# Kernel tuning notes

Measured on AMD Instinct MI355X. Metric: run time of the kernel, lower is better.

## Reference

```python
import jax, jax.numpy as jnp
import numpy as np

IN_F = 1024
OUT_F = 1024

def setup_inputs() -> dict:
    key = jax.random.key(0)
    ks = jax.random.split(key, 7)
    s = 1.0 / np.sqrt(IN_F)
    x = jax.random.normal(ks[0], (4, 2048, IN_F), dtype=jnp.float32)
    Wq = jax.random.uniform(ks[1], (OUT_F, IN_F), jnp.float32, -s, s)
    bq = jax.random.uniform(ks[2], (OUT_F,), jnp.float32, -s, s)
    Wk = jax.random.uniform(ks[3], (OUT_F, IN_F), jnp.float32, -s, s)
    bk = jax.random.uniform(ks[4], (OUT_F,), jnp.float32, -s, s)
    Wv = jax.random.uniform(ks[5], (OUT_F, IN_F), jnp.float32, -s, s)
    bv = jax.random.uniform(ks[6], (OUT_F,), jnp.float32, -s, s)
    return {"x": x, "Wq": Wq, "bq": bq, "Wk": Wk, "bk": bk, "Wv": Wv, "bv": bv}

def reference(x, Wq, bq, Wk, bk, Wv, bv):
    # Projector: ReLU(Linear(x))
    q = jax.nn.relu(jnp.einsum('bsd,od->bso', x, Wq) + bq)  # [B,S,O]
    k = jax.nn.relu(jnp.einsum('bsd,od->bso', x, Wk) + bk)
    v = jax.nn.relu(jnp.einsum('bsd,od->bso', x, Wv) + bv)
    logits = jnp.einsum('bio,bko->bik', q, k)  # unscaled QK^T, [B,S,S]
    scores = jax.nn.softmax(logits, axis=-1)
    out = jnp.einsum('bik,bko->bio', scores, v)
    return out
```

## Files before the change

### kernel.cpp

```cpp
#include <hip/hip_runtime.h>
#include <hip/hip_bf16.h>


#define SEQ 2048
#define DIM 1024
#define NB 4
#define MTOT (NB * SEQ)

typedef __attribute__((ext_vector_type(8))) short frag_ab;
typedef __attribute__((ext_vector_type(16))) float frag_c16;

__device__ __forceinline__ ushort f2bf(float f) {
    union { float f; unsigned u; } x; x.f = f;
    unsigned r = x.u + 0x7fffu + ((x.u >> 16) & 1u);
    return (ushort)(r >> 16);
}

typedef __attribute__((address_space(1))) const unsigned int guint;
typedef __attribute__((address_space(3))) unsigned int luint;

__device__ __forceinline__ void gld_lds16(const void* g, void* l) {
    __builtin_amdgcn_global_load_lds((guint*)g, (luint*)l, 16, 0, 0);
}

__device__ __forceinline__ void gemm_tiles(
    const ushort* __restrict__ A, size_t lda,
    const ushort* __restrict__ B, size_t ldb, int K,
    ushort* As, ushort* Bs, frag_c16 (&acc)[2][2])
{
    const int tid  = threadIdx.x;
    const int wave = tid >> 6;
    const int lane = tid & 63;
    const int l32  = lane & 31;
    const int half = lane >> 5;
    const int sr = wave * 16 + (lane >> 2);
    const int sc = lane & 3;
    const int wm = (wave & 1) * 64;
    const int wn = (wave >> 1) * 64;

    for (int k0 = 0; k0 < K; k0 += 32) {
        #pragma unroll
        for (int j = 0; j < 2; ++j) {
            int row = j * 64 + sr;
            int cg  = sc ^ ((row >> 1) & 3);
            ushort* la = As + (j * 64 + wave * 16) * 32;
            ushort* lb = Bs + (j * 64 + wave * 16) * 32;
            gld_lds16(A + (size_t)row * lda + k0 + cg * 8, la);
            gld_lds16(B + (size_t)row * ldb + k0 + cg * 8, lb);
        }
        __syncthreads();
        frag_ab af[2][2], bfr[2][2];
        #pragma unroll
        for (int mi = 0; mi < 2; ++mi) {
            int row = wm + mi * 32 + l32;
            int sw = (row >> 1) & 3;
            #pragma unroll
            for (int h = 0; h < 2; ++h) {
                int c = (h * 2 + half) ^ sw;
                af[mi][h] = *(const frag_ab*)&As[row * 32 + c * 8];
            }
        }
        #pragma unroll
        for (int ni = 0; ni < 2; ++ni) {
            int row = wn + ni * 32 + l32;
            int sw = (row >> 1) & 3;
            #pragma unroll
            for (int h = 0; h < 2; ++h) {
                int c = (h * 2 + half) ^ sw;
                bfr[ni][h] = *(const frag_ab*)&Bs[row * 32 + c * 8];
            }
        }
        #pragma unroll
        for (int h = 0; h < 2; ++h)
            #pragma unroll
            for (int mi = 0; mi < 2; ++mi)
                #pragma unroll
                for (int ni = 0; ni < 2; ++ni)
                    acc[mi][ni] = __builtin_amdgcn_mfma_f32_32x32x16_bf16(
                        af[mi][h], bfr[ni][h], acc[mi][ni], 0, 0, 0);
        __syncthreads();
    }
}


#define NX4 (MTOT * DIM / 4)
#define NW4 (DIM * DIM / 4)
__global__ __launch_bounds__(256) void cvt_kernel(
    const float* __restrict__ x,
    const float* __restrict__ Wq, const float* __restrict__ Wk,
    const float* __restrict__ Wv,
    ushort* __restrict__ xb, ushort* __restrict__ Wb)
{
    size_t i = (size_t)blockIdx.x * 256 + threadIdx.x;
    const float* src; ushort* dst; size_t idx;
    if (i < NX4) { src = x; dst = xb; idx = i; }
    else {
        size_t j = i - NX4;
        int w = (int)(j >> 18);
        idx = j & (NW4 - 1);
        src = w == 0 ? Wq : (w == 1 ? Wk : Wv);
        dst = Wb + (size_t)w * DIM * DIM;
    }
    float4 f = ((const float4*)src)[idx];
    ushort4 u; u.x = f2bf(f.x); u.y = f2bf(f.y); u.z = f2bf(f.z); u.w = f2bf(f.w);
    ((ushort4*)dst)[idx] = u;
}

__global__ __launch_bounds__(256) void qkv_kernel(
    const ushort* __restrict__ xb, const ushort* __restrict__ Wb,
    const float* __restrict__ bq, const float* __restrict__ bk,
    const float* __restrict__ bv,
    ushort* __restrict__ q, ushort* __restrict__ k, ushort* __restrict__ v)
{
    const float* bias; ushort* out;
    if (blockIdx.z == 0)      { bias = bq; out = q; }
    else if (blockIdx.z == 1) { bias = bk; out = k; }
    else                      { bias = bv; out = v; }
    const ushort* W = Wb + (size_t)blockIdx.z * DIM * DIM;

    __shared__ ushort As[128 * 32];
    __shared__ ushort Bs[128 * 32];

    const int tid  = threadIdx.x;
    const int wave = tid >> 6;
    const int lane = tid & 63;
    const int l32  = lane & 31;
    const int half = lane >> 5;
    const int m0 = blockIdx.x * 128;
    const int n0 = blockIdx.y * 128;
    const int wm = (wave & 1) * 64;
    const int wn = (wave >> 1) * 64;

    frag_c16 acc[2][2] = {};
    gemm_tiles(xb + (size_t)m0 * DIM, DIM, W + (size_t)n0 * DIM, DIM, DIM,
               As, Bs, acc);

    #pragma unroll
    for (int ni = 0; ni < 2; ++ni) {
        int col = n0 + wn + ni * 32 + l32;
        float bb = bias[col];
        #pragma unroll
        for (int mi = 0; mi < 2; ++mi)
            #pragma unroll
            for (int r = 0; r < 16; ++r) {
                int row = m0 + wm + mi * 32 + (r & 3) + 8 * (r >> 2) + 4 * half;
                float val = acc[mi][ni][r] + bb;
                val = val > 0.0f ? val : 0.0f;
                out[(size_t)row * DIM + col] = f2bf(val);
            }
    }
}

__global__ __launch_bounds__(256) void transpose_v(
    const ushort* __restrict__ v, ushort* __restrict__ vt)
{
    __shared__ ushort T[64][72];
    const int bz = blockIdx.z;
    const int s0 = blockIdx.x * 64;
    const int o0 = blockIdx.y * 64;
    const int t  = threadIdx.x;

    #pragma unroll
    for (int p = 0; p < 4; ++p) {
        int sl = p * 16 + (t >> 4);
        int o4 = (t & 15) * 4;
        ushort4 u = *(const ushort4*)&v[(size_t)(bz * SEQ + s0 + sl) * DIM + o0 + o4];
        *(ushort4*)&T[sl][o4] = u;
    }
    __syncthreads();
    #pragma unroll
    for (int p = 0; p < 4; ++p) {
        int ol = p * 16 + (t >> 4);
        int s4 = (t & 15) * 4;
        ushort4 u;
        u.x = T[s4 + 0][ol]; u.y = T[s4 + 1][ol];
        u.z = T[s4 + 2][ol]; u.w = T[s4 + 3][ol];
        *(ushort4*)&vt[(size_t)(bz * DIM + o0 + ol) * SEQ + s0 + s4] = u;
    }
}

__global__ __launch_bounds__(256) void qk_kernel(
    const ushort* __restrict__ q, const ushort* __restrict__ kk,
    float* __restrict__ logits)
{
    __shared__ ushort As[128 * 32];
    __shared__ ushort Bs[128 * 32];

    const int tid  = threadIdx.x;
    const int wave = tid >> 6;
    const int lane = tid & 63;
    const int l32  = lane & 31;
    const int half = lane >> 5;
    const int bz = blockIdx.z;
    const int m0 = blockIdx.x * 128;
    const int n0 = blockIdx.y * 128;
    const int wm = (wave & 1) * 64;
    const int wn = (wave >> 1) * 64;
    const size_t base = (size_t)bz * SEQ;

    frag_c16 acc[2][2] = {};
    gemm_tiles(q + (base + m0) * DIM, DIM, kk + (base + n0) * DIM, DIM, DIM,
               As, Bs, acc);

    #pragma unroll
    for (int mi = 0; mi < 2; ++mi)
        #pragma unroll
        for (int r = 0; r < 16; ++r) {
            int row = m0 + wm + mi * 32 + (r & 3) + 8 * (r >> 2) + 4 * half;
            #pragma unroll
            for (int ni = 0; ni < 2; ++ni) {
                int col = n0 + wn + ni * 32 + l32;
                logits[(base + row) * SEQ + col] = acc[mi][ni][r];
            }
        }
}

__global__ __launch_bounds__(256) void softmax_kernel(float* __restrict__ logits)
{
    float* p = logits + (size_t)blockIdx.x * SEQ;
    const int t = threadIdx.x;
    const int wave = t >> 6, lane = t & 63;

    float4 a = ((const float4*)p)[t];
    float4 b = ((const float4*)p)[t + 256];

    float m = fmaxf(fmaxf(fmaxf(a.x, a.y), fmaxf(a.z, a.w)),
                    fmaxf(fmaxf(b.x, b.y), fmaxf(b.z, b.w)));
    #pragma unroll
    for (int off = 32; off; off >>= 1) m = fmaxf(m, __shfl_down(m, off, 64));

    __shared__ float red[4];
    if (lane == 0) red[wave] = m;
    __syncthreads();
    m = fmaxf(fmaxf(red[0], red[1]), fmaxf(red[2], red[3]));

    a.x = __expf(a.x - m); a.y = __expf(a.y - m);
    a.z = __expf(a.z - m); a.w = __expf(a.w - m);
    b.x = __expf(b.x - m); b.y = __expf(b.y - m);
    b.z = __expf(b.z - m); b.w = __expf(b.w - m);

    float s = (a.x + a.y + a.z + a.w) + (b.x + b.y + b.z + b.w);
    #pragma unroll
    for (int off = 32; off; off >>= 1) s += __shfl_down(s, off, 64);
    __syncthreads();
    if (lane == 0) red[wave] = s;
    __syncthreads();
    s = red[0] + red[1] + red[2] + red[3];
    float inv = 1.0f / s;

    ushort* o = (ushort*)p;
    ushort4 u0, u1;
    u0.x = f2bf(a.x * inv); u0.y = f2bf(a.y * inv);
    u0.z = f2bf(a.z * inv); u0.w = f2bf(a.w * inv);
    u1.x = f2bf(b.x * inv); u1.y = f2bf(b.y * inv);
    u1.z = f2bf(b.z * inv); u1.w = f2bf(b.w * inv);
    ((ushort4*)o)[t]       = u0;
    ((ushort4*)o)[t + 256] = u1;
}

__global__ __launch_bounds__(256) void pv_kernel(
    const ushort* __restrict__ probs, const ushort* __restrict__ vt,
    float* __restrict__ out)
{
    __shared__ ushort As[128 * 32];
    __shared__ ushort Bs[128 * 32];

    const int tid  = threadIdx.x;
    const int wave = tid >> 6;
    const int lane = tid & 63;
    const int l32  = lane & 31;
    const int half = lane >> 5;
    const int bz = blockIdx.z;
    const int m0 = blockIdx.x * 128;
    const int n0 = blockIdx.y * 128;
    const int wm = (wave & 1) * 64;
    const int wn = (wave >> 1) * 64;

    frag_c16 acc[2][2] = {};
    gemm_tiles(probs + ((size_t)(bz * SEQ + m0)) * 4096, 4096,
               vt + ((size_t)(bz * DIM + n0)) * SEQ, SEQ, SEQ,
               As, Bs, acc);

    #pragma unroll
    for (int mi = 0; mi < 2; ++mi)
        #pragma unroll
        for (int r = 0; r < 16; ++r) {
            int row = m0 + wm + mi * 32 + (r & 3) + 8 * (r >> 2) + 4 * half;
            #pragma unroll
            for (int ni = 0; ni < 2; ++ni) {
                int col = n0 + wn + ni * 32 + l32;
                out[((size_t)(bz * SEQ + row)) * DIM + col] = acc[mi][ni][r];
            }
        }
}

extern "C" void kernel_launch(void* const* d_in, const int* in_sizes, int n_in,
                              void* d_out, int out_size, void* d_ws, size_t ws_size,
                              hipStream_t stream)
{
    const float* x  = (const float*)d_in[0];
    const float* Wq = (const float*)d_in[1];
    const float* bq = (const float*)d_in[2];
    const float* Wk = (const float*)d_in[3];
    const float* bk = (const float*)d_in[4];
    const float* Wv = (const float*)d_in[5];
    const float* bv = (const float*)d_in[6];
    float* out = (float*)d_out;

    char* ws = (char*)d_ws;
    ushort* q      = (ushort*)(ws);
    ushort* kk     = (ushort*)(ws + ((size_t)16 << 20));
    ushort* v      = (ushort*)(ws + ((size_t)32 << 20));
    ushort* vt     = (ushort*)(ws + ((size_t)48 << 20));
    float*  logits = (float*) (ws + ((size_t)64 << 20));
    ushort* xb     = (ushort*)(ws + ((size_t)64 << 20));
    ushort* Wb     = (ushort*)(ws + ((size_t)80 << 20));

    cvt_kernel<<<dim3((NX4 + 3 * NW4) / 256), 256, 0, stream>>>(
        x, Wq, Wk, Wv, xb, Wb);

    qkv_kernel<<<dim3(MTOT / 128, DIM / 128, 3), 256, 0, stream>>>(
        xb, Wb, bq, bk, bv, q, kk, v);
    transpose_v<<<dim3(SEQ / 64, DIM / 64, NB), 256, 0, stream>>>(v, vt);
    qk_kernel<<<dim3(SEQ / 128, SEQ / 128, NB), 256, 0, stream>>>(q, kk, logits);
    softmax_kernel<<<NB * SEQ, 256, 0, stream>>>(logits);
    pv_kernel<<<dim3(SEQ / 128, DIM / 128, NB), 256, 0, stream>>>(
        (const ushort*)logits, vt, out);
}
```

Before: 277.0 us.

## Replace GEMM core with 256x256 double-buffered 8-wave pipelined tiles and split-K PV

Replaces the 128x128, K=32 tile GEMM with a 256x256 tile, K=64 step routine. It uses 8 waves, double-buffered LDS, staged async global-to-LDS loads with vmcnt waits, and interleaved fragment loads and MFMA phases under raised priority. The goal is to overlap memory traffic with MFMA work and raise data reuse per tile. The PV GEMM is split in two along K and combined with atomicAdd into an output zeroed by a memset, to keep enough blocks in flight after the larger tiles shrink the grid. The cost is more LDS and registers per block, atomic traffic, and sensitivity to the hand-written barrier and vmcnt ordering.

```diff
diff --git a/kernel.cpp b/kernel.cpp
--- a/kernel.cpp
+++ b/kernel.cpp
@@ -23,62 +23,112 @@
     __builtin_amdgcn_global_load_lds((guint*)g, (luint*)l, 16, 0, 0);
 }
 
-__device__ __forceinline__ void gemm_tiles(
+__device__ __forceinline__ void bar() {
+    asm volatile("" ::: "memory");
+    __builtin_amdgcn_s_barrier();
+    asm volatile("" ::: "memory");
+}
+
+#define VMCNT4 asm volatile("s_waitcnt vmcnt(4)" ::: "memory")
+
+#define TSZ (256 * 64)
+
+__device__ __forceinline__ void stage_half(const ushort* __restrict__ P,
+                                           size_t ld, int k0, ushort* dst,
+                                           int wave, int lane)
+{
+    const int rin = lane >> 3;
+    const int cp  = lane & 7;
+    const int cl  = cp ^ rin;
+    #pragma unroll
+    for (int g = 0; g < 4; ++g) {
+        int qc  = g * 8 + wave;
+        int row = qc * 8 + rin;
+        gld_lds16(P + (size_t)row * ld + k0 + cl * 8, dst + qc * 512);
+    }
+}
+
+__device__ __forceinline__ frag_ab ldfrag(const ushort* S, int row, int ks,
+                                          int half)
+{
+    int pc = (ks * 2 + half) ^ (row & 7);
+    return *(const frag_ab*)&S[row * 64 + pc * 8];
+}
+
+__device__ __forceinline__ void load_frags(frag_ab (&f)[2][4], const ushort* S,
+                                           int r0, int l32, int half)
+{
+    #pragma unroll
+    for (int i = 0; i < 2; ++i)
+        #pragma unroll
+        for (int ks = 0; ks < 4; ++ks)
+            f[i][ks] = ldfrag(S, r0 + i * 32 + l32, ks, half);
+}
+
+template<int MP>
+__device__ __forceinline__ void mfma_phase(frag_c16 (&acc)[4][2],
+                                           const frag_ab (&af)[2][4],
+                                           const frag_ab (&bf)[2][4])
+{
+    __builtin_amdgcn_s_setprio(1);
+    #pragma unroll
+    for (int ks = 0; ks < 4; ++ks)
+        #pragma unroll
+        for (int mi = 0; mi < 2; ++mi)
+            #pragma unroll
+            for (int ni = 0; ni < 2; ++ni)
+                acc[MP * 2 + mi][ni] = __builtin_amdgcn_mfma_f32_32x32x16_bf16(
+                    af[mi][ks], bf[ni][ks], acc[MP * 2 + mi][ni], 0, 0, 0);
+    __builtin_amdgcn_s_setprio(0);
+}
+
+__device__ __forceinline__ void gemm256(
     const ushort* __restrict__ A, size_t lda,
     const ushort* __restrict__ B, size_t ldb, int K,
-    ushort* As, ushort* Bs, frag_c16 (&acc)[2][2])
+    ushort (&As)[2][TSZ], ushort (&Bs)[2][TSZ], frag_c16 (&acc)[4][2])
 {
     const int tid  = threadIdx.x;
     const int wave = tid >> 6;
     const int lane = tid & 63;
     const int l32  = lane & 31;
     const int half = lane >> 5;
-    const int sr = wave * 16 + (lane >> 2);
-    const int sc = lane & 3;
-    const int wm = (wave & 1) * 64;
-    const int wn = (wave >> 1) * 64;
-
-    for (int k0 = 0; k0 < K; k0 += 32) {
-        #pragma unroll
-        for (int j = 0; j < 2; ++j) {
-            int row = j * 64 + sr;
-            int cg  = sc ^ ((row >> 1) & 3);
-            ushort* la = As + (j * 64 + wave * 16) * 32;
-            ushort* lb = Bs + (j * 64 + wave * 16) * 32;
-            gld_lds16(A + (size_t)row * lda + k0 + cg * 8, la);
-            gld_lds16(B + (size_t)row * ldb + k0 + cg * 8, lb);
-        }
-        __syncthreads();
-        frag_ab af[2][2], bfr[2][2];
-        #pragma unroll
-        for (int mi = 0; mi < 2; ++mi) {
-            int row = wm + mi * 32 + l32;
-            int sw = (row >> 1) & 3;
-            #pragma unroll
-            for (int h = 0; h < 2; ++h) {
-                int c = (h * 2 + half) ^ sw;
-                af[mi][h] = *(const frag_ab*)&As[row * 32 + c * 8];
-            }
-        }
-        #pragma unroll
-        for (int ni = 0; ni < 2; ++ni) {
-            int row = wn + ni * 32 + l32;
-            int sw = (row >> 1) & 3;
-            #pragma unroll
-            for (int h = 0; h < 2; ++h) {
-                int c = (h * 2 + half) ^ sw;
-                bfr[ni][h] = *(const frag_ab*)&Bs[row * 32 + c * 8];
-            }
-        }
-        #pragma unroll
-        for (int h = 0; h < 2; ++h)
-            #pragma unroll
-            for (int mi = 0; mi < 2; ++mi)
-                #pragma unroll
-                for (int ni = 0; ni < 2; ++ni)
-                    acc[mi][ni] = __builtin_amdgcn_mfma_f32_32x32x16_bf16(
-                        af[mi][h], bfr[ni][h], acc[mi][ni], 0, 0, 0);
-        __syncthreads();
+    const int wm   = (wave >> 2) * 128;
+    const int wn   = (wave & 3) * 64;
+
+    stage_half(B, ldb, 0,  Bs[0], wave, lane);
+    stage_half(A, lda, 0,  As[0], wave, lane);
+    stage_half(B, ldb, 64, Bs[1], wave, lane);
+    VMCNT4;
+    __builtin_amdgcn_s_barrier();
+    asm volatile("" ::: "memory");
+
+    const int nkt = K >> 6;
+    for (int kt = 0; kt < nkt; kt += 2) {
+        frag_ab bfe[2][4], bfo[2][4], af[2][4];
+        load_frags(bfe, Bs[0], wn, l32, half);
+        load_frags(af,  As[0], wm, l32, half);
+        stage_half(A, lda, (kt + 1) * 64, As[1], wave, lane);
+        bar();
+        mfma_phase<0>(acc, af, bfe);
+        bar();
+        load_frags(af, As[0], wm + 64, l32, half);
+        stage_half(B, ldb, (kt + 2) * 64, Bs[0], wave, lane);
+        bar();
+        mfma_phase<1>(acc, af, bfe);
+        VMCNT4;
+        bar();
+        load_frags(bfo, Bs[1], wn, l32, half);
+        load_frags(af,  As[1], wm, l32, half);
+        stage_half(A, lda, (kt + 2) * 64, As[0], wave, lane);
+        bar();
+        mfma_phase<0>(acc, af, bfo);
+        bar();
+        load_frags(af, As[1], wm + 64, l32, half);
+        stage_half(B, ldb, (kt + 3) * 64, Bs[1], wave, lane);
+        bar();
+        mfma_phase<1>(acc, af, bfo);
+        VMCNT4;
+        bar();
     }
 }
 
@@ -106,41 +156,42 @@
     ((ushort4*)dst)[idx] = u;
 }
 
-__global__ __launch_bounds__(256) void qkv_kernel(
+__global__ __launch_bounds__(512, 2) void qkv_kernel(
     const ushort* __restrict__ xb, const ushort* __restrict__ Wb,
     const float* __restrict__ bq, const float* __restrict__ bk,
     const float* __restrict__ bv,
-    ushort* __restrict__ q, ushort* __restrict__ k, ushort* __restrict__ v)
-{
+    ushort* __restrict__ q, ushort* __restrict__ kk, ushort* __restrict__ v)
+{
+    __shared__ ushort As[2][TSZ];
+    __shared__ ushort Bs[2][TSZ];
+
     const float* bias; ushort* out;
     if (blockIdx.z == 0)      { bias = bq; out = q; }
-    else if (blockIdx.z == 1) { bias = bk; out = k; }
+    else if (blockIdx.z == 1) { bias = bk; out = kk; }
     else                      { bias = bv; out = v; }
     const ushort* W = Wb + (size_t)blockIdx.z * DIM * DIM;
 
-    __shared__ ushort As[128 * 32];
-    __shared__ ushort Bs[128 * 32];
+    const int m0 = blockIdx.x * 256;
+    const int n0 = blockIdx.y * 256;
+
+    frag_c16 acc[4][2] = {};
+    gemm256(xb + (size_t)m0 * DIM, DIM, W + (size_t)n0 * DIM, DIM, DIM,
+            As, Bs, acc);
 
     const int tid  = threadIdx.x;
     const int wave = tid >> 6;
     const int lane = tid & 63;
     const int l32  = lane & 31;
     const int half = lane >> 5;
-    const int m0 = blockIdx.x * 128;
-    const int n0 = blockIdx.y * 128;
-    const int wm = (wave & 1) * 64;
-    const int wn = (wave >> 1) * 64;
-
-    frag_c16 acc[2][2] = {};
-    gemm_tiles(xb + (size_t)m0 * DIM, DIM, W + (size_t)n0 * DIM, DIM, DIM,
-               As, Bs, acc);
+    const int wm   = (wave >> 2) * 128;
+    const int wn   = (wave & 3) * 64;
 
     #pragma unroll
     for (int ni = 0; ni < 2; ++ni) {
         int col = n0 + wn + ni * 32 + l32;
         float bb = bias[col];
         #pragma unroll
-        for (int mi = 0; mi < 2; ++mi)
+        for (int mi = 0; mi < 4; ++mi)
             #pragma unroll
             for (int r = 0; r < 16; ++r) {
                 int row = m0 + wm + mi * 32 + (r & 3) + 8 * (r >> 2) + 4 * half;
@@ -179,31 +230,32 @@
     }
 }
 
-__global__ __launch_bounds__(256) void qk_kernel(
+__global__ __launch_bounds__(512, 2) void qk_kernel(
     const ushort* __restrict__ q, const ushort* __restrict__ kk,
     float* __restrict__ logits)
 {
-    __shared__ ushort As[128 * 32];
-    __shared__ ushort Bs[128 * 32];
+    __shared__ ushort As[2][TSZ];
+    __shared__ ushort Bs[2][TSZ];
+
+    const int bz = blockIdx.z;
+    const int m0 = blockIdx.x * 256;
+    const int n0 = blockIdx.y * 256;
+    const size_t base = (size_t)bz * SEQ;
+
+    frag_c16 acc[4][2] = {};
+    gemm256(q + (base + m0) * DIM, DIM, kk + (base + n0) * DIM, DIM, DIM,
+            As, Bs, acc);
 
     const int tid  = threadIdx.x;
     const int wave = tid >> 6;
     const int lane = tid & 63;
     const int l32  = lane & 31;
     const int half = lane >> 5;
-    const int bz = blockIdx.z;
-    const int m0 = blockIdx.x * 128;
-    const int n0 = blockIdx.y * 128;
-    const int wm = (wave & 1) * 64;
-    const int wn = (wave >> 1) * 64;
-    const size_t base = (size_t)bz * SEQ;
-
-    frag_c16 acc[2][2] = {};
-    gemm_tiles(q + (base + m0) * DIM, DIM, kk + (base + n0) * DIM, DIM, DIM,
-               As, Bs, acc);
-
-    #pragma unroll
-    for (int mi = 0; mi < 2; ++mi)
+    const int wm   = (wave >> 2) * 128;
+    const int wn   = (wave & 3) * 64;
+
+    #pragma unroll
+    for (int mi = 0; mi < 4; ++mi)
         #pragma unroll
         for (int r = 0; r < 16; ++r) {
             int row = m0 + wm + mi * 32 + (r & 3) + 8 * (r >> 2) + 4 * half;
@@ -258,38 +310,41 @@
     ((ushort4*)o)[t + 256] = u1;
 }
 
-__global__ __launch_bounds__(256) void pv_kernel(
+__global__ __launch_bounds__(512, 2) void pv_kernel(
     const ushort* __restrict__ probs, const ushort* __restrict__ vt,
     float* __restrict__ out)
 {
-    __shared__ ushort As[128 * 32];
-    __shared__ ushort Bs[128 * 32];
+    __shared__ ushort As[2][TSZ];
+    __shared__ ushort Bs[2][TSZ];
+
+    const int bz = blockIdx.z >> 1;
+    const int kh = blockIdx.z & 1;
+    const int m0 = blockIdx.x * 256;
+    const int n0 = blockIdx.y * 256;
+
+    frag_c16 acc[4][2] = {};
+    gemm256(probs + ((size_t)(bz * SEQ + m0)) * 4096 + kh * 1024, 4096,
+            vt + ((size_t)(bz * DIM + n0)) * SEQ + kh * 1024, SEQ, 1024,
+            As, Bs, acc);
 
     const int tid  = threadIdx.x;
     const int wave = tid >> 6;
     const int lane = tid & 63;
     const int l32  = lane & 31;
     const int half = lane >> 5;
-    const int bz = blockIdx.z;
-    const int m0 = blockIdx.x * 128;
-    const int n0 = blockIdx.y * 128;
-    const int wm = (wave & 1) * 64;
-    const int wn = (wave >> 1) * 64;
-
-    frag_c16 acc[2][2] = {};
-    gemm_tiles(probs + ((size_t)(bz * SEQ + m0)) * 4096, 4096,
-               vt + ((size_t)(bz * DIM + n0)) * SEQ, SEQ, SEQ,
-               As, Bs, acc);
-
-    #pragma unroll
-    for (int mi = 0; mi < 2; ++mi)
+    const int wm   = (wave >> 2) * 128;
+    const int wn   = (wave & 3) * 64;
+
+    #pragma unroll
+    for (int mi = 0; mi < 4; ++mi)
         #pragma unroll
         for (int r = 0; r < 16; ++r) {
             int row = m0 + wm + mi * 32 + (r & 3) + 8 * (r >> 2) + 4 * half;
             #pragma unroll
             for (int ni = 0; ni < 2; ++ni) {
                 int col = n0 + wn + ni * 32 + l32;
-                out[((size_t)(bz * SEQ + row)) * DIM + col] = acc[mi][ni][r];
+                atomicAdd(&out[((size_t)(bz * SEQ + row)) * DIM + col],
+                          acc[mi][ni][r]);
             }
         }
 }
@@ -316,14 +371,16 @@
     ushort* xb     = (ushort*)(ws + ((size_t)64 << 20));
     ushort* Wb     = (ushort*)(ws + ((size_t)80 << 20));
 
+    hipMemsetAsync(out, 0, (size_t)MTOT * DIM * sizeof(float), stream);
+
     cvt_kernel<<<dim3((NX4 + 3 * NW4) / 256), 256, 0, stream>>>(
         x, Wq, Wk, Wv, xb, Wb);
 
-    qkv_kernel<<<dim3(MTOT / 128, DIM / 128, 3), 256, 0, stream>>>(
+    qkv_kernel<<<dim3(MTOT / 256, DIM / 256, 3), 512, 0, stream>>>(
         xb, Wb, bq, bk, bv, q, kk, v);
     transpose_v<<<dim3(SEQ / 64, DIM / 64, NB), 256, 0, stream>>>(v, vt);
-    qk_kernel<<<dim3(SEQ / 128, SEQ / 128, NB), 256, 0, stream>>>(q, kk, logits);
+    qk_kernel<<<dim3(SEQ / 256, SEQ / 256, NB), 512, 0, stream>>>(q, kk, logits);
     softmax_kernel<<<NB * SEQ, 256, 0, stream>>>(logits);
-    pv_kernel<<<dim3(SEQ / 128, DIM / 128, NB), 256, 0, stream>>>(
+    pv_kernel<<<dim3(SEQ / 256, DIM / 256, NB * 2), 512, 0, stream>>>(
         (const ushort*)logits, vt, out);
 }
```

Measured after the change: 323.0 us. 16.6% more time.
